# Kernel optimization log

Hardware: AMD Instinct MI355X
Metric: run time of the kernel (lower is better)

Reference implementation:

```python
import jax, jax.numpy as jnp
import numpy as np
from jax import lax

IC, OC, KS, HYP = 16, 16, 3, 128
BS, D = 4, 96

def setup_inputs() -> dict:
    key = jax.random.key(0)
    ks = jax.random.split(key, 6)
    x = jax.random.normal(ks[0], (BS, IC, D, D, D), dtype=jnp.float32)
    hyp_tensor = jax.random.normal(ks[1], (BS, HYP), dtype=jnp.float32)
    Wk = jax.random.normal(ks[2], (KS*KS*KS*IC*OC, HYP), dtype=jnp.float32) * 0.02
    bk = jax.random.normal(ks[3], (KS*KS*KS*IC*OC,), dtype=jnp.float32) * 0.02
    Wb = jax.random.normal(ks[4], (OC, HYP), dtype=jnp.float32) * 0.02
    bb = jax.random.normal(ks[5], (OC,), dtype=jnp.float32) * 0.02
    return {"x": x, "hyp_tensor": hyp_tensor, "Wk": Wk, "bk": bk, "Wb": Wb, "bb": bb}

def reference(x, hyp_tensor, Wk, bk, Wb, bb):
    bs = x.shape[0]
    # hypernetwork: per-sample kernels and biases (torch Linear: y = h @ W.T + b)
    kernel = (hyp_tensor @ Wk.T + bk).reshape(bs, OC, IC, KS, KS, KS)
    bias = hyp_tensor @ Wb.T + bb                      # [bs, OC]
    # per-sample conv == grouped conv with groups = bs
    xg = x.reshape(1, bs * IC, D, D, D)                # [1, bs*IC, D,H,W]
    kg = kernel.reshape(bs * OC, IC, KS, KS, KS)       # [bs*OC, IC, k,k,k]
    out = lax.conv_general_dilated(
        xg, kg,
        window_strides=(1, 1, 1),
        padding=[(1, 1)] * 3,
        feature_group_count=bs,
        dimension_numbers=("NCDHW", "OIDHW", "NCDHW"),
    )
    out = out.reshape(bs, OC, D, D, D) + bias[:, :, None, None, None]
    return out
```

## Files before the change

### kernel.cpp

```cpp
#include <hip/hip_runtime.h>

#define Dm 96
#define PL (Dm*Dm*Dm)
#define ICn 16
#define OCn 16
#define HYPn 128
#define BSn 4
#define NG 15
#define FRAG_ELEMS (NG*64*8)

#define XP 98
#define ROWB (XP*32)
#define PLANEB (XP*ROWB)
#define SAMPB ((size_t)XP*PLANEB)
#define XT_TOTAL ((size_t)4*SAMPB)

typedef float   f32x4  __attribute__((ext_vector_type(4)));
typedef __bf16  bf16x8 __attribute__((ext_vector_type(8)));

__device__ __forceinline__ unsigned short f2bf(float f) {
    unsigned u = __builtin_bit_cast(unsigned, f);
    u = (u + 0x7FFFu + ((u >> 16) & 1u)) >> 16;
    return (unsigned short)u;
}

__global__ __launch_bounds__(256)
void prep_kernel(const float* __restrict__ x, char* __restrict__ xT,
                 const float* __restrict__ hyp, const float* __restrict__ Wk,
                 const float* __restrict__ bk, unsigned short* __restrict__ kwf,
                 const float* __restrict__ Wb, const float* __restrict__ bb,
                 float* __restrict__ bias, int boff)
{
    int blk = blockIdx.x + boff;
    int tid = threadIdx.x;

    if (blk < 1536) {
        int yq = blk & 3;
        int z  = (blk >> 2) % Dm;
        int b  = (blk >> 2) / Dm;
        char* xTp = xT + (size_t)b*SAMPB + (size_t)(z+1)*PLANEB;
        const float* xb = x + (size_t)b*ICn*PL + (size_t)z*Dm*Dm;

        for (int t = tid; t < 1152; t += 256) {
            int ich = t & 1;
            int r   = t >> 1;
            int q = r % 24, yy = r / 24;
            int y = yq*24 + yy;
            const float* g = xb + (size_t)(ich*8)*PL + y*Dm + 4*q;
            f32x4 ld[8];
#pragma unroll
            for (int ic = 0; ic < 8; ++ic)
                ld[ic] = *(const f32x4*)(g + (size_t)ic*PL);
            char* w = xTp + (size_t)(y+1)*ROWB + (size_t)(1 + 4*q)*32 + ich*16;
#pragma unroll
            for (int xi = 0; xi < 4; ++xi) {
                bf16x8 v;
#pragma unroll
                for (int e = 0; e < 8; ++e) v[e] = (__bf16)ld[e][xi];
                *(bf16x8*)(w + xi*32) = v;
            }
        }
        bf16x8 z8;
#pragma unroll
        for (int i = 0; i < 8; ++i) z8[i] = (__bf16)0.f;
        for (int t = tid; t < 96; t += 256) {
            int half = t & 1, side = (t >> 1) & 1, yy = t >> 2;
            int y = yq*24 + yy;
            *(bf16x8*)(xTp + (size_t)(y+1)*ROWB + (size_t)(side ? 97 : 0)*32 + half*16) = z8;
        }
        if (yq == 0 || yq == 3) {
            char* w0 = xTp + (size_t)(yq == 0 ? 0 : 97)*ROWB;
            for (int t = tid; t < XP*2; t += 256)
                *(bf16x8*)(w0 + (size_t)t*16) = z8;
        }
        return;
    }
    if (blk < 1544) {
        int idx = blk - 1536;
        int b = idx >> 1, zb = idx & 1;
        char* p = xT + (size_t)b*SAMPB + (size_t)(zb ? 97 : 0)*PLANEB;
        f32x4 z4 = {0.f,0.f,0.f,0.f};
        for (int i = tid; i < PLANEB/16; i += 256)
            *(f32x4*)(p + (size_t)i*16) = z4;
        return;
    }
    if (blk < 1664) {
        int t = (blk - 1544) * 256 + tid;
        int j    = t & 7;
        int lane = (t >> 3) & 63;
        int rest = t >> 9;
        int grp  = rest % NG;
        int b    = rest / NG;
        int oc = lane & 15, hi = lane >> 4;
        int ty = grp / 5, g = grp % 5;
        int cl = hi >> 1;
        int ic = (hi & 1) * 8 + j;
        int c  = 2 * g + cl;
        float acc = 0.f;
        if (c < 9) {
            int tz = c / 3, tx = c % 3;
            int r = (oc * ICn + ic) * 27 + (tz * 9 + ty * 3 + tx);
            const float4* w = (const float4*)(Wk + (long)r * HYPn);
            const float4* h = (const float4*)(hyp + (long)b * HYPn);
            acc = bk[r];
#pragma unroll
            for (int q = 0; q < HYPn / 4; ++q) {
                float4 a = h[q], cc = w[q];
                acc += a.x * cc.x + a.y * cc.y + a.z * cc.z + a.w * cc.w;
            }
        }
        kwf[t] = f2bf(acc);
        return;
    }
    if (tid < 64) {
        int b = tid >> 4, oc = tid & 15;
        const float4* w = (const float4*)(Wb + (long)oc * HYPn);
        const float4* h = (const float4*)(hyp + (long)b * HYPn);
        float acc = bb[oc];
#pragma unroll
        for (int q = 0; q < HYPn / 4; ++q) {
            float4 a = h[q], c = w[q];
            acc += a.x * c.x + a.y * c.y + a.z * c.z + a.w * c.w;
        }
        bias[tid] = acc;
    }
}

#define ZT 4
#define YT 8
#define XT 16
#define ZL 6
#define YL 10
#define XL 18
#define SSTR 32
#define SPN (ZL*YL*XL)
#define LPTS 1088
#define LDSB (LPTS*SSTR)
#define NDMA 34
#define NT 6
#define ZCH (ZT*NT)

__device__ constexpr int coff(int c) {
    return ((c / 3) * YL * XL + (c % 3)) * SSTR;
}

__device__ __forceinline__ void dma_tile(const char* org, char* buf,
                                         const unsigned* goff, int wz, int lane)
{
#pragma unroll
    for (int m = 0; m < 9; ++m) {
        if (wz + 4*m < NDMA) {
            int i = wz + 4*m;
            __builtin_amdgcn_global_load_lds(
                (const __attribute__((address_space(1))) unsigned int*)(org + goff[m]),
                (__attribute__((address_space(3))) unsigned int*)(buf + i*1024 + lane*16),
                16, 0, 0);
        }
    }
}

__global__ __launch_bounds__(256, 2)
void conv_dma_kernel(const char* __restrict__ xT, const unsigned short* __restrict__ kwf,
                     const float* __restrict__ bias, float* __restrict__ out)
{
    __shared__ __align__(16) char smem[2*LDSB];

    const int NB = BSn * 6 * 12 * 4;
    int raw = blockIdx.x;
    int u = (raw & 7) * (NB/8) + (raw >> 3);

    int tx = u % 6;  u /= 6;
    int ty = u % 12; u /= 12;
    int zc = u % 4;
    int b  = u / 4;
    int x0 = tx*XT, y0 = ty*YT, zbase = zc*ZCH;

    int tid  = threadIdx.x;
    int lane = tid & 63;
    int wz   = tid >> 6;

    const unsigned short* kwb = kwf + (long)b * FRAG_ELEMS;
    f32x4 afr[NG];
#pragma unroll
    for (int grp = 0; grp < NG; ++grp) {
        afr[grp] = *(const f32x4*)(kwb + (grp * 64 + lane) * 8);
        asm volatile("" : "+v"(afr[grp]));
    }

    unsigned goff[9];
#pragma unroll
    for (int m = 0; m < 9; ++m) {
        int i = wz + 4*m;
        if (i >= NDMA) i = NDMA - 1;
        int flat = i*64 + lane;
        int p = flat >> 1;  if (p > 1079) p = 1079;
        int half = flat & 1;
        int lz = p / (YL*XL), r = p % (YL*XL), ly = r / XL, lx = r % XL;
        goff[m] = (unsigned)(lz*PLANEB + ly*ROWB + lx*32 + half*16);
    }

    int n   = lane & 15;
    int hi  = lane >> 4;
    int cl  = hi >> 1;
    int ich = hi & 1;

    int addr_g[5];
#pragma unroll
    for (int g = 0; g < 5; ++g) {
        int c = 2 * g + cl;
        if (c > 8) c = 8;
        addr_g[g] = ((wz * YL) * XL + n) * SSTR + ich * 16 + coff(c);
    }

    float4 bv = *(const float4*)(bias + b * OCn + hi * 4);

    const char* xsamp = xT + (size_t)b*SAMPB + (size_t)y0*ROWB + (size_t)x0*32;

    char* buf0 = smem;
    char* buf1 = smem + LDSB;

    dma_tile(xsamp + (size_t)zbase*PLANEB, buf0, goff, wz, lane);
    __syncthreads();

#pragma unroll
    for (int t = 0; t < NT; ++t) {
        char* cur = (t & 1) ? buf1 : buf0;
        char* nxt = (t & 1) ? buf0 : buf1;
        int ztile = zbase + t*ZT;

        if (t + 1 < NT) {
            dma_tile(xsamp + (size_t)(ztile + ZT)*PLANEB, nxt, goff, wz, lane);
            __builtin_amdgcn_sched_barrier(0);
        }

        f32x4 acc[YT];
#pragma unroll
        for (int yy = 0; yy < YT; ++yy) acc[yy] = (f32x4){0.f,0.f,0.f,0.f};

#pragma unroll
        for (int p = 0; p < YL; ++p) {
            bf16x8 F[5];
#pragma unroll
            for (int g = 0; g < 5; ++g)
                F[g] = *(const bf16x8*)(cur + addr_g[g] + p * (XL * SSTR));
#pragma unroll
            for (int tyk = 0; tyk < 3; ++tyk) {
                int yy = p - tyk;
                if (yy >= 0 && yy < YT) {
#pragma unroll
                    for (int g = 0; g < 5; ++g)
                        acc[yy] = __builtin_amdgcn_mfma_f32_16x16x32_bf16(
                            __builtin_bit_cast(bf16x8, afr[tyk * 5 + g]), F[g], acc[yy], 0, 0, 0);
                }
            }
        }

        int zo = ztile + wz;
#pragma unroll
        for (int yy = 0; yy < YT; ++yy) {
            int yo = y0 + yy;
            long obase = ((((long)b * OCn + hi * 4) * Dm + zo) * Dm + yo) * Dm + x0 + n;
#pragma unroll
            for (int r = 0; r < 4; ++r)
                out[obase + (long)r * PL] = acc[yy][r] + ((const float*)&bv)[r];
        }

        if (t + 1 < NT) {
            asm volatile("s_waitcnt vmcnt(32)" ::: "memory");
            __builtin_amdgcn_s_barrier();
            __builtin_amdgcn_sched_barrier(0);
        }
    }
}

__global__ __launch_bounds__(256, 4)
void conv_fb_kernel(const float* __restrict__ x, const unsigned short* __restrict__ kwf,
                    const float* __restrict__ bias, float* __restrict__ out)
{
    __shared__ __align__(16) char smem[SPN*SSTR];

    const int NXT = Dm / XT, NYT = Dm / YT, NZT = Dm / ZT;
    int raw = blockIdx.x;
    int bid = (raw & 7) * ((BSn * NXT * NYT * NZT) / 8) + (raw >> 3);

    int txi = bid % NXT; bid /= NXT;
    int tyi = bid % NYT; bid /= NYT;
    int tzi = bid % NZT;
    int b   = bid / NZT;
    int x0 = txi * XT, y0 = tyi * YT, z0 = tzi * ZT;

    int tid  = threadIdx.x;
    int lane = tid & 63;
    int wz   = tid >> 6;

    const float* xb = x + (long)b * ICn * PL;

    for (int t = tid; t < 480; t += 256) {
        int xq  = t & 3;
        int ich = (t >> 2) & 1;
        int row = t >> 3;
        int ly = row % YL, lz = row / YL;
        int gz = z0 - 1 + lz, gy = y0 - 1 + ly;
        int gx = x0 + 4 * xq;
        bf16x8 v[4];
        if ((unsigned)gz < (unsigned)Dm && (unsigned)gy < (unsigned)Dm) {
            const float* g = xb + (long)(ich * 8) * PL + ((long)gz * Dm + gy) * Dm + gx;
#pragma unroll
            for (int q = 0; q < 8; ++q) {
                f32x4 p = *(const f32x4*)(g + (long)q * PL);
                v[0][q] = (__bf16)p.x; v[1][q] = (__bf16)p.y;
                v[2][q] = (__bf16)p.z; v[3][q] = (__bf16)p.w;
            }
        } else {
#pragma unroll
            for (int xi = 0; xi < 4; ++xi)
#pragma unroll
                for (int q = 0; q < 8; ++q) v[xi][q] = (__bf16)0.f;
        }
        int sp = (lz * YL + ly) * XL + (1 + 4 * xq);
#pragma unroll
        for (int xi = 0; xi < 4; ++xi)
            *(bf16x8*)(smem + (sp + xi) * SSTR + ich * 16) = v[xi];
    }
    for (int t = tid; t < 240; t += 256) {
        int s   = t & 1;
        int ich = (t >> 1) & 1;
        int row = t >> 2;
        int ly = row % YL, lz = row / YL;
        int gz = z0 - 1 + lz, gy = y0 - 1 + ly;
        int lx = s ? (XL - 1) : 0;
        int gx = x0 - 1 + lx;
        bf16x8 v;
        if ((unsigned)gz < (unsigned)Dm && (unsigned)gy < (unsigned)Dm &&
            (unsigned)gx < (unsigned)Dm) {
            const float* g = xb + (long)(ich * 8) * PL + ((long)gz * Dm + gy) * Dm + gx;
#pragma unroll
            for (int q = 0; q < 8; ++q) v[q] = (__bf16)g[(long)q * PL];
        } else {
#pragma unroll
            for (int q = 0; q < 8; ++q) v[q] = (__bf16)0.f;
        }
        int sp = (lz * YL + ly) * XL + lx;
        *(bf16x8*)(smem + sp * SSTR + ich * 16) = v;
    }

    const unsigned short* kwb = kwf + (long)b * FRAG_ELEMS;
    f32x4 afr[NG];
#pragma unroll
    for (int grp = 0; grp < NG; ++grp) {
        afr[grp] = *(const f32x4*)(kwb + (grp * 64 + lane) * 8);
        asm volatile("" : "+v"(afr[grp]));
    }

    __syncthreads();

    int n   = lane & 15;
    int hi  = lane >> 4;
    int cl  = hi >> 1;
    int ich = hi & 1;

    int addr_g[5];
#pragma unroll
    for (int g = 0; g < 5; ++g) {
        int c = 2 * g + cl;
        if (c > 8) c = 8;
        addr_g[g] = ((wz * YL) * XL + n) * SSTR + ich * 16 + coff(c);
    }

    f32x4 acc[YT];
#pragma unroll
    for (int yy = 0; yy < YT; ++yy) acc[yy] = (f32x4){0.f, 0.f, 0.f, 0.f};

#pragma unroll
    for (int p = 0; p < YL; ++p) {
        bf16x8 F[5];
#pragma unroll
        for (int g = 0; g < 5; ++g)
            F[g] = *(const bf16x8*)(smem + addr_g[g] + p * (XL * SSTR));
#pragma unroll
        for (int tyk = 0; tyk < 3; ++tyk) {
            int yy = p - tyk;
            if (yy >= 0 && yy < YT) {
#pragma unroll
                for (int g = 0; g < 5; ++g)
                    acc[yy] = __builtin_amdgcn_mfma_f32_16x16x32_bf16(
                        __builtin_bit_cast(bf16x8, afr[tyk * 5 + g]), F[g], acc[yy], 0, 0, 0);
            }
        }
    }

    float4 bv = *(const float4*)(bias + b * OCn + hi * 4);
    int zo = z0 + wz;
#pragma unroll
    for (int yy = 0; yy < YT; ++yy) {
        int yo = y0 + yy;
        long obase = ((((long)b * OCn + hi * 4) * Dm + zo) * Dm + yo) * Dm + x0 + n;
#pragma unroll
        for (int r = 0; r < 4; ++r)
            out[obase + (long)r * PL] = acc[yy][r] + ((const float*)&bv)[r];
    }
}

extern "C" void kernel_launch(void* const* d_in, const int* in_sizes, int n_in,
                              void* d_out, int out_size, void* d_ws, size_t ws_size,
                              hipStream_t stream)
{
    const float* x   = (const float*)d_in[0];
    const float* hyp = (const float*)d_in[1];
    const float* Wk  = (const float*)d_in[2];
    const float* bk  = (const float*)d_in[3];
    const float* Wb  = (const float*)d_in[4];
    const float* bb  = (const float*)d_in[5];
    float* out = (float*)d_out;

    const size_t need = XT_TOTAL + 61440 + 256;
    if (ws_size >= need) {
        char* xT = (char*)d_ws;
        unsigned short* kwf = (unsigned short*)(xT + XT_TOTAL);
        float* biasp = (float*)(xT + XT_TOTAL + 61440);

        hipLaunchKernelGGL(prep_kernel, dim3(1665), dim3(256), 0, stream,
                           x, xT, hyp, Wk, bk, kwf, Wb, bb, biasp, 0);
        hipLaunchKernelGGL(conv_dma_kernel, dim3(BSn * 6 * 12 * 4), dim3(256), 0, stream,
                           xT, kwf, biasp, out);
    } else {
        unsigned short* kwf = (unsigned short*)d_ws;
        float* biasp = (float*)((char*)d_ws + (size_t)BSn * FRAG_ELEMS * 2);

        hipLaunchKernelGGL(prep_kernel, dim3(121), dim3(256), 0, stream,
                           x, (char*)d_ws, hyp, Wk, bk, kwf, Wb, bb, biasp, 1544);
        hipLaunchKernelGGL(conv_fb_kernel, dim3(BSn * 6 * 12 * 24), dim3(256), 0, stream,
                           x, kwf, biasp, out);
    }
}
```

Measured before the change: 190.1 us.

## Replace LDS double-buffered DMA conv with direct global/L2 loads per wave

The main conv kernel drops the LDS staging via global_load_lds and its barriers. Each 64-thread block now reads bf16 input fragments directly from the padded transposed buffer, relying on L1/L2 for reuse, and software-pipelines the row loads two rows ahead in registers. The grid grows to many single-wave blocks, each covering 4 z-planes. This removes LDS traffic and synchronisation but repeats global loads for the overlapping halo across the 3x3x3 taps, which could make the kernel bound on cache bandwidth.

```diff
diff --git a/kernel.cpp b/kernel.cpp
--- a/kernel.cpp
+++ b/kernel.cpp
@@ -126,58 +126,26 @@
     }
 }
 
-#define ZT 4
 #define YT 8
 #define XT 16
-#define ZL 6
 #define YL 10
-#define XL 18
-#define SSTR 32
-#define SPN (ZL*YL*XL)
-#define LPTS 1088
-#define LDSB (LPTS*SSTR)
-#define NDMA 34
-#define NT 6
-#define ZCH (ZT*NT)
-
-__device__ constexpr int coff(int c) {
-    return ((c / 3) * YL * XL + (c % 3)) * SSTR;
-}
-
-__device__ __forceinline__ void dma_tile(const char* org, char* buf,
-                                         const unsigned* goff, int wz, int lane)
+#define NZW 4
+
+__global__ __launch_bounds__(64, 2)
+void conv_l2_kernel(const char* __restrict__ xT, const unsigned short* __restrict__ kwf,
+                    const float* __restrict__ bias, float* __restrict__ out)
 {
-#pragma unroll
-    for (int m = 0; m < 9; ++m) {
-        if (wz + 4*m < NDMA) {
-            int i = wz + 4*m;
-            __builtin_amdgcn_global_load_lds(
-                (const __attribute__((address_space(1))) unsigned int*)(org + goff[m]),
-                (__attribute__((address_space(3))) unsigned int*)(buf + i*1024 + lane*16),
-                16, 0, 0);
-        }
-    }
-}
-
-__global__ __launch_bounds__(256, 2)
-void conv_dma_kernel(const char* __restrict__ xT, const unsigned short* __restrict__ kwf,
-                     const float* __restrict__ bias, float* __restrict__ out)
-{
-    __shared__ __align__(16) char smem[2*LDSB];
-
-    const int NB = BSn * 6 * 12 * 4;
+    const int NU = BSn * (Dm/NZW) * (Dm/YT) * (Dm/XT);
     int raw = blockIdx.x;
-    int u = (raw & 7) * (NB/8) + (raw >> 3);
+    int u = (raw & 7) * (NU/8) + (raw >> 3);
 
     int tx = u % 6;  u /= 6;
     int ty = u % 12; u /= 12;
-    int zc = u % 4;
-    int b  = u / 4;
-    int x0 = tx*XT, y0 = ty*YT, zbase = zc*ZCH;
-
-    int tid  = threadIdx.x;
-    int lane = tid & 63;
-    int wz   = tid >> 6;
+    int zq = u % 24;
+    int b  = u / 24;
+    int x0 = tx*XT, y0 = ty*YT, z0 = zq*NZW;
+
+    int lane = threadIdx.x;
 
     const unsigned short* kwb = kwf + (long)b * FRAG_ELEMS;
     f32x4 afr[NG];
@@ -185,18 +153,6 @@
     for (int grp = 0; grp < NG; ++grp) {
         afr[grp] = *(const f32x4*)(kwb + (grp * 64 + lane) * 8);
         asm volatile("" : "+v"(afr[grp]));
-    }
-
-    unsigned goff[9];
-#pragma unroll
-    for (int m = 0; m < 9; ++m) {
-        int i = wz + 4*m;
-        if (i >= NDMA) i = NDMA - 1;
-        int flat = i*64 + lane;
-        int p = flat >> 1;  if (p > 1079) p = 1079;
-        int half = flat & 1;
-        int lz = p / (YL*XL), r = p % (YL*XL), ly = r / XL, lx = r % XL;
-        goff[m] = (unsigned)(lz*PLANEB + ly*ROWB + lx*32 + half*16);
     }
 
     int n   = lane & 15;
@@ -204,45 +160,42 @@
     int cl  = hi >> 1;
     int ich = hi & 1;
 
-    int addr_g[5];
+    unsigned vboff[5];
 #pragma unroll
     for (int g = 0; g < 5; ++g) {
-        int c = 2 * g + cl;
+        int c = 2*g + cl;
         if (c > 8) c = 8;
-        addr_g[g] = ((wz * YL) * XL + n) * SSTR + ich * 16 + coff(c);
+        vboff[g] = (unsigned)((c/3)*PLANEB + (n + (c%3))*32 + ich*16);
     }
 
     float4 bv = *(const float4*)(bias + b * OCn + hi * 4);
 
-    const char* xsamp = xT + (size_t)b*SAMPB + (size_t)y0*ROWB + (size_t)x0*32;
-
-    char* buf0 = smem;
-    char* buf1 = smem + LDSB;
-
-    dma_tile(xsamp + (size_t)zbase*PLANEB, buf0, goff, wz, lane);
-    __syncthreads();
-
-#pragma unroll
-    for (int t = 0; t < NT; ++t) {
-        char* cur = (t & 1) ? buf1 : buf0;
-        char* nxt = (t & 1) ? buf0 : buf1;
-        int ztile = zbase + t*ZT;
-
-        if (t + 1 < NT) {
-            dma_tile(xsamp + (size_t)(ztile + ZT)*PLANEB, nxt, goff, wz, lane);
-            __builtin_amdgcn_sched_barrier(0);
-        }
+    const char* xw0 = xT + (size_t)b*SAMPB + (size_t)z0*PLANEB
+                         + (size_t)y0*ROWB + (size_t)x0*32;
+
+#pragma unroll 1
+    for (int zi = 0; zi < NZW; ++zi) {
+        const char* xw = xw0 + (size_t)zi*PLANEB;
+
+        auto loadp = [&](int P, bf16x8* F) {
+#pragma unroll
+            for (int g = 0; g < 5; ++g)
+                F[g] = *(const bf16x8*)(xw + vboff[g] + (unsigned)(P*ROWB));
+        };
 
         f32x4 acc[YT];
 #pragma unroll
         for (int yy = 0; yy < YT; ++yy) acc[yy] = (f32x4){0.f,0.f,0.f,0.f};
 
+        bf16x8 Fa[5], Fb[5], Fc[5];
+        loadp(0, Fa);
+        loadp(1, Fb);
+
 #pragma unroll
         for (int p = 0; p < YL; ++p) {
-            bf16x8 F[5];
-#pragma unroll
-            for (int g = 0; g < 5; ++g)
-                F[g] = *(const bf16x8*)(cur + addr_g[g] + p * (XL * SSTR));
+            bf16x8* cur = (p % 3 == 0) ? Fa : (p % 3 == 1) ? Fb : Fc;
+            bf16x8* nx2 = (p % 3 == 0) ? Fc : (p % 3 == 1) ? Fa : Fb;
+            if (p + 2 < YL) loadp(p + 2, nx2);
 #pragma unroll
             for (int tyk = 0; tyk < 3; ++tyk) {
                 int yy = p - tyk;
@@ -250,27 +203,31 @@
 #pragma unroll
                     for (int g = 0; g < 5; ++g)
                         acc[yy] = __builtin_amdgcn_mfma_f32_16x16x32_bf16(
-                            __builtin_bit_cast(bf16x8, afr[tyk * 5 + g]), F[g], acc[yy], 0, 0, 0);
+                            __builtin_bit_cast(bf16x8, afr[tyk*5 + g]), cur[g], acc[yy], 0, 0, 0);
                 }
             }
         }
 
-        int zo = ztile + wz;
+        int z = z0 + zi;
 #pragma unroll
         for (int yy = 0; yy < YT; ++yy) {
             int yo = y0 + yy;
-            long obase = ((((long)b * OCn + hi * 4) * Dm + zo) * Dm + yo) * Dm + x0 + n;
+            long obase = ((((long)b * OCn + hi * 4) * Dm + z) * Dm + yo) * Dm + x0 + n;
 #pragma unroll
             for (int r = 0; r < 4; ++r)
                 out[obase + (long)r * PL] = acc[yy][r] + ((const float*)&bv)[r];
         }
-
-        if (t + 1 < NT) {
-            asm volatile("s_waitcnt vmcnt(32)" ::: "memory");
-            __builtin_amdgcn_s_barrier();
-            __builtin_amdgcn_sched_barrier(0);
-        }
-    }
+    }
+}
+
+#define ZT 4
+#define ZL 6
+#define XL 18
+#define SSTR 32
+#define SPN (ZL*YL*XL)
+
+__device__ constexpr int coff(int c) {
+    return ((c / 3) * YL * XL + (c % 3)) * SSTR;
 }
 
 __global__ __launch_bounds__(256, 4)
@@ -421,7 +378,7 @@
 
         hipLaunchKernelGGL(prep_kernel, dim3(1665), dim3(256), 0, stream,
                            x, xT, hyp, Wk, bk, kwf, Wb, bb, biasp, 0);
-        hipLaunchKernelGGL(conv_dma_kernel, dim3(BSn * 6 * 12 * 4), dim3(256), 0, stream,
+        hipLaunchKernelGGL(conv_l2_kernel, dim3(BSn * 24 * 12 * 6), dim3(64), 0, stream,
                            xT, kwf, biasp, out);
     } else {
         unsigned short* kwf = (unsigned short*)d_ws;
```

New measurement: 255.9 us. +34.6%, slower.
